# Kernel optimization log

Hardware: AMD Instinct MI355X
Metric: run time of the kernel (lower is better)

The kernel has to match this reference:

```python
import jax, jax.numpy as jnp
import numpy as np

D_IN = 1024
D_OUT = 1024

def setup_inputs() -> dict:
    key = jax.random.key(0)
    kx, kq, kk, kv = jax.random.split(key, 4)
    X = jax.random.normal(kx, (4, 2048, D_IN), dtype=jnp.float32)
    s = 1.0 / np.sqrt(D_IN)
    Wq = jax.random.uniform(kq, (D_IN, D_OUT), jnp.float32, -s, s)
    Wk = jax.random.uniform(kk, (D_IN, D_OUT), jnp.float32, -s, s)
    Wv = jax.random.uniform(kv, (D_IN, D_OUT), jnp.float32, -s, s)
    return {"X": X, "Wq": Wq, "Wk": Wk, "Wv": Wv}

def reference(X, Wq, Wk, Wv):
    # X: [b, s, d_in]; W*: [d_in, d_out] (torch Linear weight transposed)
    B, S, _ = X.shape
    q = jnp.einsum('bsd,de->bse', X, Wq)
    k = jnp.einsum('bsd,de->bse', X, Wk)
    v = jnp.einsum('bsd,de->bse', X, Wv)
    scores = jnp.einsum('bqe,bke->bqk', q, k)  # [b, s, s]
    causal = jnp.triu(jnp.ones((S, S), dtype=bool), k=1)
    scores = jnp.where(causal, -jnp.inf, scores)
    weights = jax.nn.softmax(scores / jnp.sqrt(jnp.asarray(k.shape[-1], scores.dtype)), axis=-1)
    # dropout p=0.0 (eval) -> identity
    return jnp.einsum('bqk,bke->bqe', weights, v)
```

## Files before the change

kernel.cpp:

```cpp
#include <hip/hip_runtime.h>
#include <cstdint>
#include <cmath>

typedef unsigned short u16;
typedef u16   u16x4  __attribute__((ext_vector_type(4)));
typedef u16   u16x8  __attribute__((ext_vector_type(8)));
typedef __bf16 bf16x8 __attribute__((ext_vector_type(8)));
typedef float f32x4  __attribute__((ext_vector_type(4)));

__device__ __forceinline__ u16 f2bf(float f) {
    uint32_t u = __builtin_bit_cast(uint32_t, f);
    u += 0x7fffu + ((u >> 16) & 1u);
    return (u16)(u >> 16);
}
__device__ __forceinline__ float bf2f(u16 v) {
    uint32_t u = ((uint32_t)v) << 16;
    return __builtin_bit_cast(float, u);
}
__device__ __forceinline__ void gload_lds16(const u16* g, u16* l) {
    __builtin_amdgcn_global_load_lds((const __attribute__((address_space(1))) void*)g,
                                     (__attribute__((address_space(3))) void*)l,
                                     16, 0, 0);
}

__global__ __launch_bounds__(256) void prep_kernel(const float* __restrict__ X,
                                                   const float* __restrict__ Wq,
                                                   const float* __restrict__ Wk,
                                                   const float* __restrict__ Wv,
                                                   u16* __restrict__ Xb,
                                                   u16* __restrict__ Wt,
                                                   float* __restrict__ rowsum) {
    __shared__ u16 tile[64 * 72];
    typedef float f4 __attribute__((ext_vector_type(4)));
    const int bid = blockIdx.x;
    if (bid < 2048) {
        const int base = bid * 1024 + threadIdx.x;
#pragma unroll
        for (int k = 0; k < 4; k++) {
            const int idx = base + k * 256;
            f4 f = ((const f4*)X)[idx];
            u16x4 o;
            o[0] = f2bf(f[0]); o[1] = f2bf(f[1]); o[2] = f2bf(f[2]); o[3] = f2bf(f[3]);
            ((u16x4*)Xb)[idx] = o;
        }
        return;
    }
    if (bid == 2816) {
        f32x4 z = {0.f, 0.f, 0.f, 0.f};
        f32x4* p = (f32x4*)rowsum;
#pragma unroll
        for (int k = 0; k < 8; k++) p[k * 256 + threadIdx.x] = z;
        return;
    }
    const int id = bid - 2048;
    const int z = id >> 8, rem = id & 255;
    const float* W = (z == 0) ? Wq : (z == 1) ? Wk : Wv;
    u16* out = Wt + ((size_t)z << 20);
    const int nt = (rem & 15) * 64, kt = (rem >> 4) * 64;
    const int t = threadIdx.x, r = t >> 2, cq = (t & 3) * 16;
    const float* src = W + (size_t)(kt + r) * 1024 + nt + cq;
#pragma unroll
    for (int q = 0; q < 4; q++) {
        f4 f = ((const f4*)src)[q];
        tile[r * 72 + cq + q * 4 + 0] = f2bf(f[0]);
        tile[r * 72 + cq + q * 4 + 1] = f2bf(f[1]);
        tile[r * 72 + cq + q * 4 + 2] = f2bf(f[2]);
        tile[r * 72 + cq + q * 4 + 3] = f2bf(f[3]);
    }
    __syncthreads();
    u16x8 o0, o1;
#pragma unroll
    for (int e = 0; e < 8; e++) { o0[e] = tile[(cq + e) * 72 + r]; o1[e] = tile[(cq + 8 + e) * 72 + r]; }
    u16* dst = out + (size_t)(nt + r) * 1024 + kt + cq;
    *(u16x8*)dst = o0;
    *(u16x8*)(dst + 8) = o1;
}

__global__ __launch_bounds__(512, 2) void qkv_gemm_kernel(const u16* __restrict__ Xb,
                                                          const u16* __restrict__ Wt,
                                                          u16* __restrict__ QKV) {
    __shared__ u16 lds[65536];
    const int bid = blockIdx.x;
    const int xcd = bid & 7, slot = bid >> 3;
    const int m0 = (xcd * 8 + (slot >> 3)) << 7;
    const int n0 = (slot & 7) << 7;

    const int tid = (int)threadIdx.x;
    const int w = tid >> 6, l = tid & 63;
    const int wm = w >> 2, wn = w & 3;

    const int srow = w * 16 + (l >> 3);
    const int scol = ((l & 7) ^ ((l >> 3) & 7)) * 8;
    const u16* gA  = Xb + (size_t)(m0 + srow) * 1024 + scol;
    const u16* gB0 = Wt + (size_t)(n0 + srow) * 1024 + scol;
    const u16* gB1 = gB0 + ((size_t)1 << 20);
    const u16* gB2 = gB0 + ((size_t)2 << 20);
    u16* const sA = lds + w * 1024;
    u16* const sB = lds + 16384 + w * 1024;

    const int c0 = ((l >> 4) ^ (l & 7)) * 8;
    const u16* const pa_ = lds + (wm * 64 + (l & 15)) * 64;
    const u16* const pb_ = lds + 16384 + (wn * 32 + (l & 15)) * 64;

    f32x4 acc[3][4][2] = {};
    bf16x8 a[4][2], b[2][2];

#define MFMA_ __builtin_amdgcn_mfma_f32_16x16x32_bf16
#define STG_A(P, T) \
    gload_lds16(gA + (size_t)(T) * 64,                    sA + (P) * 8192); \
    gload_lds16(gA + (size_t)(T) * 64 + (size_t)8 * 1024, sA + (P) * 8192 + 512);
#define STG_B(P, Z, GB, T) \
    gload_lds16(GB + (size_t)(T) * 64,                    sB + (Z) * 16384 + (P) * 8192); \
    gload_lds16(GB + (size_t)(T) * 64 + (size_t)8 * 1024, sB + (Z) * 16384 + (P) * 8192 + 512);
#define LD_A(P) \
    _Pragma("unroll") for (int m_ = 0; m_ < 4; m_++) { \
        a[m_][0] = *(const bf16x8*)(pa_ + (P) * 8192 + m_ * 1024 + c0); \
        a[m_][1] = *(const bf16x8*)(pa_ + (P) * 8192 + m_ * 1024 + (c0 ^ 32)); \
    }
#define LD_B(P, Z) \
    _Pragma("unroll") for (int n_ = 0; n_ < 2; n_++) { \
        b[n_][0] = *(const bf16x8*)(pb_ + (Z) * 16384 + (P) * 8192 + n_ * 1024 + c0); \
        b[n_][1] = *(const bf16x8*)(pb_ + (Z) * 16384 + (P) * 8192 + n_ * 1024 + (c0 ^ 32)); \
    }
#define MM(Z) \
    _Pragma("unroll") for (int m_ = 0; m_ < 4; m_++) { \
        _Pragma("unroll") for (int n_ = 0; n_ < 2; n_++) { \
            acc[Z][m_][n_] = MFMA_(a[m_][0], b[n_][0], acc[Z][m_][n_], 0, 0, 0); \
            acc[Z][m_][n_] = MFMA_(a[m_][1], b[n_][1], acc[Z][m_][n_], 0, 0, 0); \
        } \
    }
#define VM6 asm volatile("s_waitcnt vmcnt(6)" ::: "memory");
#define VM0 asm volatile("s_waitcnt vmcnt(0)" ::: "memory");
#define VMN
#define BAR __builtin_amdgcn_s_barrier();
#define PRIO1 __builtin_amdgcn_s_setprio(1);
#define PRIO0 __builtin_amdgcn_s_setprio(0);
#define TILE(P, S1, T1, S2, T2, VM3) \
    LD_A(P) LD_B(P, 0) \
    if (S1) { STG_B((P) ^ 1, 2, gB2, T1) } \
    BAR PRIO1 MM(0) PRIO0 BAR \
    LD_B(P, 1) \
    if (S2) { STG_A(P, T2) STG_B(P, 0, gB0, T2) } \
    BAR PRIO1 MM(1) PRIO0 BAR \
    LD_B(P, 2) \
    if (S2) { STG_B(P, 1, gB1, T2) } \
    VM3 \
    BAR PRIO1 MM(2) PRIO0 BAR

    STG_A(0, 0) STG_B(0, 0, gB0, 0) STG_B(0, 1, gB1, 0) STG_B(0, 2, gB2, 0)
    STG_A(1, 1) STG_B(1, 0, gB0, 1) STG_B(1, 1, gB1, 1)
    asm volatile("s_waitcnt vmcnt(6)" ::: "memory");
    __builtin_amdgcn_s_barrier();

#pragma unroll 1
    for (int i = 0; i < 7; ++i) {
        TILE(0, 1, 2 * i + 1, 1, 2 * i + 2, VM6)
        TILE(1, 1, 2 * i + 2, 1, 2 * i + 3, VM6)
    }
    TILE(0, 1, 15, 0, 0, VM0)
    TILE(1, 0, 0, 0, 0, VMN)

    const int row0 = m0 + wm * 64 + ((l >> 4) << 2);
    const int col0 = n0 + wn * 32 + (l & 15);
#pragma unroll
    for (int z = 0; z < 3; z++) {
        u16* C = QKV + ((size_t)z << 23);
#pragma unroll
        for (int m = 0; m < 4; m++)
#pragma unroll
            for (int r = 0; r < 4; r++) {
                u16* po = C + (size_t)(row0 + m * 16 + r) * 1024 + col0;
#pragma unroll
                for (int n = 0; n < 2; n++) po[n * 16] = f2bf(acc[z][m][n][r]);
            }
    }
#undef MFMA_
#undef STG_A
#undef STG_B
#undef LD_A
#undef LD_B
#undef MM
#undef VM6
#undef VM0
#undef VMN
#undef BAR
#undef PRIO1
#undef PRIO0
#undef TILE
}

__global__ __launch_bounds__(512, 2) void qk_tr_kernel(const u16* __restrict__ QKV,
                                                       u16* __restrict__ S,
                                                       u16* __restrict__ Vt,
                                                       float* __restrict__ rowsum) {
    __shared__ u16 lds[32768];
    const int bid = blockIdx.x;
    const int tid = (int)threadIdx.x;
    if (bid >= 544) {
        const int tile_id = (bid - 544) * 2 + (tid >> 8);
        const int t = tid & 255;
        const int b = tile_id >> 9, rem = tile_id & 511;
        const u16* src = QKV + ((size_t)2 << 23) + ((size_t)b << 21);
        u16* dst = Vt + ((size_t)b << 21);
        const int st = (rem & 31) * 64, et = (rem >> 5) * 64;
        u16 (*tile)[72] = (u16(*)[72])(lds + (tid >> 8) * 4608);
        const int r = t >> 2, cq = (t & 3) * 16;
        const u16* p = src + (size_t)(st + r) * 1024 + et + cq;
        u16x8 u0 = *(const u16x8*)p;
        u16x8 u1 = *(const u16x8*)(p + 8);
#pragma unroll
        for (int e = 0; e < 8; e++) { tile[r][cq + e] = u0[e]; tile[r][cq + 8 + e] = u1[e]; }
        __syncthreads();
        u16x8 o0, o1;
#pragma unroll
        for (int e = 0; e < 8; e++) { o0[e] = tile[cq + e][r]; o1[e] = tile[cq + 8 + e][r]; }
        u16* q = dst + (size_t)(et + r) * 2048 + st + cq;
        *(u16x8*)q = o0;
        *(u16x8*)(q + 8) = o1;
        return;
    }
    const int x = bid & 7;
    const int idx = bid >> 3;
    const int b = idx & 3;
    const int u = idx >> 2;
    int it, jt;
    if (u < 16 - x) { it = 15 - x; jt = u; }
    else            { it = x;      jt = u - (16 - x); }
    const int m0 = it * 128, n0 = jt * 128;
    const u16* Q = QKV + ((size_t)b << 21);
    const u16* K = QKV + ((size_t)1 << 23) + ((size_t)b << 21);
    u16* Sb = S + ((size_t)b << 22);
    float* rs = rowsum + (b << 11);

    const int w = tid >> 6, l = tid & 63;
    const int wm = w >> 2, wn = w & 3;
    const int srow = w * 16 + (l >> 3);
    const int scol = ((l & 7) ^ ((l >> 3) & 7)) * 8;
    const u16* gA = Q + (size_t)(m0 + srow) * 1024 + scol;
    const u16* gB = K + (size_t)(n0 + srow) * 1024 + scol;
    u16* const sA = lds + w * 1024;
    u16* const sB = lds + 16384 + w * 1024;
    const int c0 = ((l >> 4) ^ (l & 7)) * 8;
    const u16* const pa_ = lds + (wm * 64 + (l & 15)) * 64;
    const u16* const pb_ = lds + 16384 + (wn * 32 + (l & 15)) * 64;

    f32x4 acc[4][2] = {};
#define QSTG(T, BUF) \
    gload_lds16(gA + (size_t)(T) * 64,                    sA + (BUF) * 8192); \
    gload_lds16(gA + (size_t)(T) * 64 + (size_t)8 * 1024, sA + (BUF) * 8192 + 512); \
    gload_lds16(gB + (size_t)(T) * 64,                    sB + (BUF) * 8192); \
    gload_lds16(gB + (size_t)(T) * 64 + (size_t)8 * 1024, sB + (BUF) * 8192 + 512);

    QSTG(0, 0)
#pragma unroll 1
    for (int kt = 0; kt < 16; ++kt) {
        if (kt < 15) {
            QSTG(kt + 1, (kt + 1) & 1)
            asm volatile("s_waitcnt vmcnt(4)" ::: "memory");
        } else {
            asm volatile("s_waitcnt vmcnt(0)" ::: "memory");
        }
        __builtin_amdgcn_s_barrier();
        const int rb = (kt & 1) * 8192;
        bf16x8 a[4][2], bb[2][2];
#pragma unroll
        for (int m = 0; m < 4; m++) {
            a[m][0] = *(const bf16x8*)(pa_ + rb + m * 1024 + c0);
            a[m][1] = *(const bf16x8*)(pa_ + rb + m * 1024 + (c0 ^ 32));
        }
#pragma unroll
        for (int n = 0; n < 2; n++) {
            bb[n][0] = *(const bf16x8*)(pb_ + rb + n * 1024 + c0);
            bb[n][1] = *(const bf16x8*)(pb_ + rb + n * 1024 + (c0 ^ 32));
        }
        __builtin_amdgcn_s_setprio(1);
#pragma unroll
        for (int m = 0; m < 4; m++)
#pragma unroll
            for (int n = 0; n < 2; n++) {
                acc[m][n] = __builtin_amdgcn_mfma_f32_16x16x32_bf16(a[m][0], bb[n][0], acc[m][n], 0, 0, 0);
                acc[m][n] = __builtin_amdgcn_mfma_f32_16x16x32_bf16(a[m][1], bb[n][1], acc[m][n], 0, 0, 0);
            }
        __builtin_amdgcn_s_setprio(0);
        __builtin_amdgcn_s_barrier();
    }
#undef QSTG
    const float sc = 0.03125f * 1.44269504088896f;
    const bool diag = (it == jt);
    const int row0g = m0 + wm * 64 + ((l >> 4) << 2);
    const int col0g = n0 + wn * 32 + (l & 15);
#pragma unroll
    for (int m = 0; m < 4; m++)
#pragma unroll
        for (int r = 0; r < 4; r++) {
            const int row = row0g + m * 16 + r;
            u16* po = Sb + (size_t)row * 2048 + col0g;
            float psum = 0.f;
#pragma unroll
            for (int n = 0; n < 2; n++) {
                const int col = col0g + n * 16;
                const float p = (diag && col > row) ? 0.f : exp2f(acc[m][n][r] * sc);
                po[n * 16] = f2bf(p);
                psum += p;
            }
            psum += __shfl_xor(psum, 1, 64);
            psum += __shfl_xor(psum, 2, 64);
            psum += __shfl_xor(psum, 4, 64);
            psum += __shfl_xor(psum, 8, 64);
            if ((l & 15) == 0) atomicAdd(rs + row, psum);
        }
}

__device__ __forceinline__ void pv_tile128(const u16* __restrict__ Pb,
                                           const u16* __restrict__ Vb,
                                           float* __restrict__ Ob,
                                           const float* __restrict__ rs,
                                           u16* __restrict__ lds,
                                           const int it, const int n0) {
    const int tid = (int)threadIdx.x;
    const int w = tid >> 6, l = tid & 63;
    const int wm = w >> 2, wn = w & 3;
    const int nk = 2 * (it + 1);
    const int m0 = it * 128;

    const int srow = w * 16 + (l >> 3);
    const int scol = ((l & 7) ^ ((l >> 3) & 7)) * 8;
    const u16* gA = Pb + (size_t)(m0 + srow) * 2048 + scol;
    const u16* gB = Vb + (size_t)(n0 + srow) * 2048 + scol;
    u16* const sA = lds + w * 1024;
    u16* const sB = lds + 24576 + w * 1024;

    const int c0 = ((l >> 4) ^ (l & 7)) * 8;
    const u16* const pa_ = lds + (wm * 64 + (l & 15)) * 64;
    const u16* const pb_ = lds + 24576 + (wn * 32 + (l & 15)) * 64;

    f32x4 acc[4][2] = {};

#define PSTG(T, BUF) \
    gload_lds16(gA + (size_t)(T) * 64,                    sA + (BUF) * 8192); \
    gload_lds16(gA + (size_t)(T) * 64 + (size_t)8 * 2048, sA + (BUF) * 8192 + 512); \
    gload_lds16(gB + (size_t)(T) * 64,                    sB + (BUF) * 8192); \
    gload_lds16(gB + (size_t)(T) * 64 + (size_t)8 * 2048, sB + (BUF) * 8192 + 512);

    PSTG(0, 0) PSTG(1, 1)
    asm volatile("s_waitcnt vmcnt(4)" ::: "memory");
    __builtin_amdgcn_s_barrier();

    int bufR = 0, bufW = 2;
#pragma unroll 1
    for (int t = 0; t < nk; ++t) {
        bf16x8 a[4][2], b[2][2];
#pragma unroll
        for (int m = 0; m < 4; m++) {
            a[m][0] = *(const bf16x8*)(pa_ + bufR * 8192 + m * 1024 + c0);
            a[m][1] = *(const bf16x8*)(pa_ + bufR * 8192 + m * 1024 + (c0 ^ 32));
        }
#pragma unroll
        for (int n = 0; n < 2; n++) {
            b[n][0] = *(const bf16x8*)(pb_ + bufR * 8192 + n * 1024 + c0);
            b[n][1] = *(const bf16x8*)(pb_ + bufR * 8192 + n * 1024 + (c0 ^ 32));
        }
        if (t < nk - 2) {
            PSTG(t + 2, bufW)
            asm volatile("s_waitcnt vmcnt(4)" ::: "memory");
        } else {
            asm volatile("s_waitcnt vmcnt(0)" ::: "memory");
        }
        __builtin_amdgcn_s_barrier();
        __builtin_amdgcn_s_setprio(1);
#pragma unroll
        for (int m = 0; m < 4; m++)
#pragma unroll
            for (int n = 0; n < 2; n++) {
                acc[m][n] = __builtin_amdgcn_mfma_f32_16x16x32_bf16(a[m][0], b[n][0], acc[m][n], 0, 0, 0);
                acc[m][n] = __builtin_amdgcn_mfma_f32_16x16x32_bf16(a[m][1], b[n][1], acc[m][n], 0, 0, 0);
            }
        __builtin_amdgcn_s_setprio(0);
        __builtin_amdgcn_s_barrier();
        bufR = (bufR == 2) ? 0 : bufR + 1;
        bufW = (bufW == 2) ? 0 : bufW + 1;
    }
#undef PSTG

    const int row0 = m0 + wm * 64 + ((l >> 4) << 2);
    const int col0 = n0 + wn * 32 + (l & 15);
#pragma unroll
    for (int m = 0; m < 4; m++) {
        const f32x4 rsv = *(const f32x4*)(rs + row0 + m * 16);
#pragma unroll
        for (int r = 0; r < 4; r++) {
            const float inv = 1.f / rsv[r];
            float* po = Ob + (size_t)(row0 + m * 16 + r) * 1024 + col0;
#pragma unroll
            for (int n = 0; n < 2; n++) po[n * 16] = acc[m][n][r] * inv;
        }
    }
}

__global__ __launch_bounds__(512, 2) void pv_gemm_kernel(const u16* __restrict__ P,
                                                         const u16* __restrict__ Vt,
                                                         float* __restrict__ O,
                                                         const float* __restrict__ rowsum) {
    __shared__ u16 lds[49152];
    const int bid = blockIdx.x;
    const int xcd = bid & 7, slot = bid >> 3;
    const int combo = xcd * 4 + (slot >> 3);
    const int n0 = (slot & 7) * 128;
    const int pair = combo >> 2, b = combo & 3;
    const u16* Pb = P + ((size_t)b << 22);
    const u16* Vb = Vt + ((size_t)b << 21);
    float* Ob = O + ((size_t)b << 21);
    const float* rb = rowsum + (b << 11);
    pv_tile128(Pb, Vb, Ob, rb, lds, 15 - pair, n0);
    pv_tile128(Pb, Vb, Ob, rb, lds, pair, n0);
}

extern "C" void kernel_launch(void* const* d_in, const int* in_sizes, int n_in,
                              void* d_out, int out_size, void* d_ws, size_t ws_size,
                              hipStream_t stream) {
    const float* X  = (const float*)d_in[0];
    const float* Wq = (const float*)d_in[1];
    const float* Wk = (const float*)d_in[2];
    const float* Wv = (const float*)d_in[3];
    float* out = (float*)d_out;

    u16* ws  = (u16*)d_ws;
    u16* Xb  = ws;
    u16* Wt  = Xb + ((size_t)1 << 23);
    u16* QKV = Wt + 3 * ((size_t)1 << 20);
    u16* S   = QKV + 3 * ((size_t)1 << 23);
    u16* Vt  = Xb;
    float* rowsum = (float*)(S + ((size_t)1 << 24));

    prep_kernel<<<2817, 256, 0, stream>>>(X, Wq, Wk, Wv, Xb, Wt, rowsum);
    qkv_gemm_kernel<<<512, 512, 0, stream>>>(Xb, Wt, QKV);
    qk_tr_kernel<<<1568, 512, 0, stream>>>(QKV, S, Vt, rowsum);
    pv_gemm_kernel<<<256, 512, 0, stream>>>(S, Vt, out, rowsum);
}
```

Baseline: 218.8 us.

## Split PV GEMM into one tile per block with double-buffered LDS

Each PV block used to process a heavy and a light causal tile pair back to back. Now 512 blocks each take a single 128-row tile, ordered so the heavy tiles launch first in phase 0 and the light ones follow. The LDS pipeline shrinks from triple to double buffering with prefetch distance one, which cuts shared memory from 96KB to 64KB per block and may allow more residency. The risk is less load-latency hiding and extra tail or scheduling imbalance, because per-block work is no longer paired.

Result: no change. 215.9 us (-1.3%).

```diff
diff --git a/kernel.cpp b/kernel.cpp
--- a/kernel.cpp
+++ b/kernel.cpp
@@ -311,74 +311,75 @@
         }
 }
 
-__device__ __forceinline__ void pv_tile128(const u16* __restrict__ Pb,
-                                           const u16* __restrict__ Vb,
-                                           float* __restrict__ Ob,
-                                           const float* __restrict__ rs,
-                                           u16* __restrict__ lds,
-                                           const int it, const int n0) {
-    const int tid = (int)threadIdx.x;
-    const int w = tid >> 6, l = tid & 63;
-    const int wm = w >> 2, wn = w & 3;
+__global__ __launch_bounds__(512, 2) void pv_gemm_kernel(const u16* __restrict__ P,
+                                                         const u16* __restrict__ Vt,
+                                                         float* __restrict__ O,
+                                                         const float* __restrict__ rowsum) {
+    __shared__ u16 lds[32768];
+    const int bid = blockIdx.x;
+    const int phase = bid >> 8, c = bid & 255;
+    const int x = c & 7;
+    const int rr = c >> 3;
+    const int b = rr >> 3, n0 = (rr & 7) * 128;
+    const int it = phase ? x : (15 - x);
     const int nk = 2 * (it + 1);
     const int m0 = it * 128;
-
+    const u16* Pb = P + ((size_t)b << 22);
+    const u16* Vb = Vt + ((size_t)b << 21);
+    float* Ob = O + ((size_t)b << 21);
+    const float* rs = rowsum + (b << 11);
+
+    const int tid = (int)threadIdx.x, w = tid >> 6, l = tid & 63;
+    const int wm = w >> 2, wn = w & 3;
     const int srow = w * 16 + (l >> 3);
     const int scol = ((l & 7) ^ ((l >> 3) & 7)) * 8;
     const u16* gA = Pb + (size_t)(m0 + srow) * 2048 + scol;
     const u16* gB = Vb + (size_t)(n0 + srow) * 2048 + scol;
     u16* const sA = lds + w * 1024;
-    u16* const sB = lds + 24576 + w * 1024;
-
+    u16* const sB = lds + 16384 + w * 1024;
     const int c0 = ((l >> 4) ^ (l & 7)) * 8;
     const u16* const pa_ = lds + (wm * 64 + (l & 15)) * 64;
-    const u16* const pb_ = lds + 24576 + (wn * 32 + (l & 15)) * 64;
+    const u16* const pb_ = lds + 16384 + (wn * 32 + (l & 15)) * 64;
 
     f32x4 acc[4][2] = {};
-
 #define PSTG(T, BUF) \
     gload_lds16(gA + (size_t)(T) * 64,                    sA + (BUF) * 8192); \
     gload_lds16(gA + (size_t)(T) * 64 + (size_t)8 * 2048, sA + (BUF) * 8192 + 512); \
     gload_lds16(gB + (size_t)(T) * 64,                    sB + (BUF) * 8192); \
     gload_lds16(gB + (size_t)(T) * 64 + (size_t)8 * 2048, sB + (BUF) * 8192 + 512);
 
-    PSTG(0, 0) PSTG(1, 1)
-    asm volatile("s_waitcnt vmcnt(4)" ::: "memory");
-    __builtin_amdgcn_s_barrier();
-
-    int bufR = 0, bufW = 2;
+    PSTG(0, 0)
 #pragma unroll 1
-    for (int t = 0; t < nk; ++t) {
-        bf16x8 a[4][2], b[2][2];
-#pragma unroll
-        for (int m = 0; m < 4; m++) {
-            a[m][0] = *(const bf16x8*)(pa_ + bufR * 8192 + m * 1024 + c0);
-            a[m][1] = *(const bf16x8*)(pa_ + bufR * 8192 + m * 1024 + (c0 ^ 32));
-        }
-#pragma unroll
-        for (int n = 0; n < 2; n++) {
-            b[n][0] = *(const bf16x8*)(pb_ + bufR * 8192 + n * 1024 + c0);
-            b[n][1] = *(const bf16x8*)(pb_ + bufR * 8192 + n * 1024 + (c0 ^ 32));
-        }
-        if (t < nk - 2) {
-            PSTG(t + 2, bufW)
+    for (int kt = 0; kt < nk; ++kt) {
+        if (kt < nk - 1) {
+            PSTG(kt + 1, (kt + 1) & 1)
             asm volatile("s_waitcnt vmcnt(4)" ::: "memory");
         } else {
             asm volatile("s_waitcnt vmcnt(0)" ::: "memory");
         }
         __builtin_amdgcn_s_barrier();
+        const int rb2 = (kt & 1) * 8192;
+        bf16x8 a[4][2], bb[2][2];
+#pragma unroll
+        for (int m = 0; m < 4; m++) {
+            a[m][0] = *(const bf16x8*)(pa_ + rb2 + m * 1024 + c0);
+            a[m][1] = *(const bf16x8*)(pa_ + rb2 + m * 1024 + (c0 ^ 32));
+        }
+#pragma unroll
+        for (int n = 0; n < 2; n++) {
+            bb[n][0] = *(const bf16x8*)(pb_ + rb2 + n * 1024 + c0);
+            bb[n][1] = *(const bf16x8*)(pb_ + rb2 + n * 1024 + (c0 ^ 32));
+        }
         __builtin_amdgcn_s_setprio(1);
 #pragma unroll
         for (int m = 0; m < 4; m++)
 #pragma unroll
             for (int n = 0; n < 2; n++) {
-                acc[m][n] = __builtin_amdgcn_mfma_f32_16x16x32_bf16(a[m][0], b[n][0], acc[m][n], 0, 0, 0);
-                acc[m][n] = __builtin_amdgcn_mfma_f32_16x16x32_bf16(a[m][1], b[n][1], acc[m][n], 0, 0, 0);
+                acc[m][n] = __builtin_amdgcn_mfma_f32_16x16x32_bf16(a[m][0], bb[n][0], acc[m][n], 0, 0, 0);
+                acc[m][n] = __builtin_amdgcn_mfma_f32_16x16x32_bf16(a[m][1], bb[n][1], acc[m][n], 0, 0, 0);
             }
         __builtin_amdgcn_s_setprio(0);
         __builtin_amdgcn_s_barrier();
-        bufR = (bufR == 2) ? 0 : bufR + 1;
-        bufW = (bufW == 2) ? 0 : bufW + 1;
     }
 #undef PSTG
 
@@ -395,24 +396,6 @@
             for (int n = 0; n < 2; n++) po[n * 16] = acc[m][n][r] * inv;
         }
     }
-}
-
-__global__ __launch_bounds__(512, 2) void pv_gemm_kernel(const u16* __restrict__ P,
-                                                         const u16* __restrict__ Vt,
-                                                         float* __restrict__ O,
-                                                         const float* __restrict__ rowsum) {
-    __shared__ u16 lds[49152];
-    const int bid = blockIdx.x;
-    const int xcd = bid & 7, slot = bid >> 3;
-    const int combo = xcd * 4 + (slot >> 3);
-    const int n0 = (slot & 7) * 128;
-    const int pair = combo >> 2, b = combo & 3;
-    const u16* Pb = P + ((size_t)b << 22);
-    const u16* Vb = Vt + ((size_t)b << 21);
-    float* Ob = O + ((size_t)b << 21);
-    const float* rb = rowsum + (b << 11);
-    pv_tile128(Pb, Vb, Ob, rb, lds, 15 - pair, n0);
-    pv_tile128(Pb, Vb, Ob, rb, lds, pair, n0);
 }
 
 extern "C" void kernel_launch(void* const* d_in, const int* in_sizes, int n_in,
@@ -435,5 +418,5 @@
     prep_kernel<<<2817, 256, 0, stream>>>(X, Wq, Wk, Wv, Xb, Wt, rowsum);
     qkv_gemm_kernel<<<512, 512, 0, stream>>>(Xb, Wt, QKV);
     qk_tr_kernel<<<1568, 512, 0, stream>>>(QKV, S, Vt, rowsum);
-    pv_gemm_kernel<<<256, 512, 0, stream>>>(S, Vt, out, rowsum);
-}
+    pv_gemm_kernel<<<512, 512, 0, stream>>>(S, Vt, out, rowsum);
+}
```
